# Kernel tuning notes

Measured on AMD Instinct MI355X. Metric: run time of the kernel, lower is better.

Reference implementation:

```python
import jax, jax.numpy as jnp
import numpy as np

N_NODES = 100000


def gcn_conv(x, edge_index, edge_weight, W, b):
    """PyG GCNConv: out = D^-1/2 (A + I) D^-1/2 X W + b (self-loop weight 1)."""
    n = x.shape[0]
    src, dst = edge_index[0], edge_index[1]
    loop = jnp.arange(n)
    src_sl = jnp.concatenate([src, loop])
    dst_sl = jnp.concatenate([dst, loop])
    ew_sl = jnp.concatenate([edge_weight, jnp.ones((n,), x.dtype)])
    deg = jax.ops.segment_sum(ew_sl, dst_sl, num_segments=n)  # [N]
    dinv = jnp.where(deg > 0, jax.lax.rsqrt(deg), 0.0)
    norm = dinv[src_sl] * ew_sl * dinv[dst_sl]  # [E+N]
    h = x @ W  # [N, out_dim] dense transform before propagation
    msg = h[src_sl] * norm[:, None]  # gather + scale, [E+N, out_dim]
    out = jax.ops.segment_sum(msg, dst_sl, num_segments=n)  # scatter-add
    return out + b


def setup_inputs() -> dict:
    key = jax.random.key(0)
    ks = jax.random.split(key, 9)
    in_dim, hidden, latent = 128, 64, 32
    n, e = N_NODES, 1600000
    x = jax.random.normal(ks[0], (n, in_dim), dtype=jnp.float32)
    edge_index = jax.random.randint(ks[1], (2, e), 0, n, dtype=jnp.int64)
    edge_weight = jax.random.uniform(ks[2], (e,), dtype=jnp.float32)
    def glorot(k, fan_in, fan_out):
        s = jnp.sqrt(6.0 / (fan_in + fan_out))
        return jax.random.uniform(k, (fan_in, fan_out), jnp.float32, -s, s)
    return {
        "x": x,
        "edge_index": edge_index,
        "edge_weight": edge_weight,
        "W1": glorot(ks[3], in_dim, hidden),
        "b1": jnp.zeros((hidden,), jnp.float32),
        "W_mu": glorot(ks[4], hidden, latent),
        "b_mu": jnp.zeros((latent,), jnp.float32),
        "W_lv": glorot(ks[5], hidden, latent),
        "b_lv": jnp.zeros((latent,), jnp.float32),
    }


def reference(x, edge_index, edge_weight, W1, b1, W_mu, b_mu, W_lv, b_lv):
    h = jax.nn.relu(gcn_conv(x, edge_index, edge_weight, W1, b1))
    mu = gcn_conv(h, edge_index, edge_weight, W_mu, b_mu)
    logvar = gcn_conv(h, edge_index, edge_weight, W_lv, b_lv)
    return (mu, logvar)
```

## Files before the change

kernel.cpp:

```cpp
#include <hip/hip_runtime.h>

static __device__ __forceinline__ float4 ld4(const float* p) { return *(const float4*)p; }
static __device__ __forceinline__ float b2f(unsigned short u) {
    return __uint_as_float((unsigned)u << 16);
}
static __device__ __forceinline__ float b2f_lo(unsigned u) { return __uint_as_float(u << 16); }
static __device__ __forceinline__ float b2f_hi(unsigned u) { return __uint_as_float(u & 0xFFFF0000u); }
static __device__ __forceinline__ unsigned short f2b(float f) {
    unsigned x = __float_as_uint(f);
    return (unsigned short)((x + 0x7FFFu + ((x >> 16) & 1u)) >> 16);
}
static __device__ __forceinline__ unsigned pk2(float lo, float hi) {
    return (unsigned)f2b(lo) | ((unsigned)f2b(hi) << 16);
}

typedef __attribute__((ext_vector_type(8))) short bf16x8;
typedef __attribute__((ext_vector_type(4))) float f32x4;

#define NPB 256
#define CAPE 5120



__global__ __launch_bounds__(256) void k_prep(const float* __restrict__ W1,
                                              const float* __restrict__ Wmu,
                                              const float* __restrict__ Wlv,
                                              unsigned short* __restrict__ Wf1,
                                              unsigned short* __restrict__ Wf2) {
    int tid = threadIdx.x;
    if (blockIdx.x == 0) {
        for (int idx = tid; idx < 2048; idx += 256) {
            int frag = idx >> 6, lane = idx & 63;
            int s = frag & 1, ct = (frag >> 1) & 3, kb = frag >> 3;
            int rA = lane & 15, g8 = (lane >> 4) * 8;
            int c = ct * 16 + rA;
            unsigned short* dstp = Wf1 + frag * 512 + lane * 8;
            for (int j = 0; j < 8; j++) {
                float wv = W1[(size_t)(kb * 32 + g8 + j) * 64 + c];
                unsigned short hi = f2b(wv);
                dstp[j] = (s == 0) ? hi : f2b(wv - b2f(hi));
            }
        }
    } else {
        for (int idx = tid; idx < 1024; idx += 256) {
            int frag = idx >> 6, lane = idx & 63;
            int s = frag & 1, ct = (frag >> 1) & 3, kb = frag >> 3;
            int rA = lane & 15, g8 = (lane >> 4) * 8;
            int c = ct * 16 + rA;
            int k0 = kb * 32 + g8;
            unsigned short* dstp = Wf2 + frag * 512 + lane * 8;
            for (int j = 0; j < 8; j++) {
                float wv = (c < 32) ? Wmu[(size_t)(k0 + j) * 32 + c]
                                    : Wlv[(size_t)(k0 + j) * 32 + (c - 32)];
                unsigned short hi = f2b(wv);
                dstp[j] = (s == 0) ? hi : f2b(wv - b2f(hi));
            }
        }
    }
}

static __device__ __forceinline__ void split8(const float* xv, bf16x8& ah, bf16x8& al) {
    #pragma unroll
    for (int j = 0; j < 8; j++) {
        unsigned u = __float_as_uint(xv[j]);
        float res = xv[j] - __uint_as_float(u & 0xFFFF0000u);
        ah[j] = (short)(u >> 16);
        al[j] = (short)(__float_as_uint(res) >> 16);
    }
}

__global__ __launch_bounds__(256) void k_fused1(const float* __restrict__ A,
                                                const unsigned short* __restrict__ Wf1,
                                                unsigned short* __restrict__ gout,
                                                const int* __restrict__ src,
                                                const int* __restrict__ dst,
                                                const float* __restrict__ ew,
                                                int* __restrict__ bin_cnt,
                                                unsigned long long* __restrict__ ebuf,
                                                int n, int E, int bb_cnt, int NB) {
    __shared__ int hist[512];
    __shared__ int hbase[512];
    int tid = threadIdx.x;

    if ((int)blockIdx.x >= bb_cnt) {
        int row0 = ((int)blockIdx.x - bb_cnt) * 128;
        int w = tid >> 6, lane = tid & 63;
        int rA = lane & 15, g8 = (lane >> 4) * 8;
        int rowa = row0 + w * 16 + rA;
        int rowb = rowa + 64;
        const float* xa = A + (size_t)min(rowa, n - 1) * 128;
        const float* xb = A + (size_t)min(rowb, n - 1) * 128;
        f32x4 acc0[4] = {{0.f,0.f,0.f,0.f},{0.f,0.f,0.f,0.f},{0.f,0.f,0.f,0.f},{0.f,0.f,0.f,0.f}};
        f32x4 acc1[4] = {{0.f,0.f,0.f,0.f},{0.f,0.f,0.f,0.f},{0.f,0.f,0.f,0.f},{0.f,0.f,0.f,0.f}};
        #pragma unroll
        for (int kb = 0; kb < 4; kb++) {
            float4 va0 = ld4(xa + kb * 32 + g8);
            float4 va1 = ld4(xa + kb * 32 + g8 + 4);
            float4 vb0 = ld4(xb + kb * 32 + g8);
            float4 vb1 = ld4(xb + kb * 32 + g8 + 4);
            float xva[8] = {va0.x, va0.y, va0.z, va0.w, va1.x, va1.y, va1.z, va1.w};
            float xvb[8] = {vb0.x, vb0.y, vb0.z, vb0.w, vb1.x, vb1.y, vb1.z, vb1.w};
            bf16x8 ahA, alA, ahB, alB;
            split8(xva, ahA, alA);
            split8(xvb, ahB, alB);
            const unsigned short* wb = Wf1 + (size_t)(kb * 8) * 512 + lane * 8;
            #pragma unroll
            for (int ct = 0; ct < 4; ct++) {
                bf16x8 bh = *(const bf16x8*)(wb + (ct * 2 + 0) * 512);
                bf16x8 bl = *(const bf16x8*)(wb + (ct * 2 + 1) * 512);
                acc0[ct] = __builtin_amdgcn_mfma_f32_16x16x32_bf16(ahA, bh, acc0[ct], 0, 0, 0);
                acc0[ct] = __builtin_amdgcn_mfma_f32_16x16x32_bf16(alA, bh, acc0[ct], 0, 0, 0);
                acc0[ct] = __builtin_amdgcn_mfma_f32_16x16x32_bf16(ahA, bl, acc0[ct], 0, 0, 0);
                acc1[ct] = __builtin_amdgcn_mfma_f32_16x16x32_bf16(ahB, bh, acc1[ct], 0, 0, 0);
                acc1[ct] = __builtin_amdgcn_mfma_f32_16x16x32_bf16(alB, bh, acc1[ct], 0, 0, 0);
                acc1[ct] = __builtin_amdgcn_mfma_f32_16x16x32_bf16(ahB, bl, acc1[ct], 0, 0, 0);
            }
        }
        int rbase = row0 + w * 16 + (lane >> 4) * 4;
        #pragma unroll
        for (int reg = 0; reg < 4; reg++) {
            int grow = rbase + reg;
            if (grow < n) {
                #pragma unroll
                for (int ct = 0; ct < 4; ct++)
                    gout[(size_t)grow * 64 + ct * 16 + rA] = f2b(acc0[ct][reg]);
            }
            int grow2 = grow + 64;
            if (grow2 < n) {
                #pragma unroll
                for (int ct = 0; ct < 4; ct++)
                    gout[(size_t)grow2 * 64 + ct * 16 + rA] = f2b(acc1[ct][reg]);
            }
        }
    } else {
        for (int j = tid; j < NB; j += 256) hist[j] = 0;
        __syncthreads();
        int e0 = (int)blockIdx.x * 4096;
        unsigned long long pk[16]; int bb[16]; int loc[16];
        #pragma unroll
        for (int j = 0; j < 16; j++) {
            int e = e0 + j * 256 + tid;
            if (e < E) {
                int s = src[e];
                int d = dst[e];
                float w = ew[e];
                bb[j] = d >> 8;
                pk[j] = ((unsigned long long)__float_as_uint(w) << 32) |
                        (unsigned)((d & (NPB - 1)) << 17) | (unsigned)s;
                loc[j] = atomicAdd(&hist[bb[j]], 1);
            } else bb[j] = -1;
        }
        __syncthreads();
        for (int j = tid; j < NB; j += 256) hbase[j] = atomicAdd(&bin_cnt[j], hist[j]);
        __syncthreads();
        #pragma unroll
        for (int j = 0; j < 16; j++) {
            if (bb[j] >= 0)
                ebuf[(size_t)bb[j] * CAPE + hbase[bb[j]] + loc[j]] = pk[j];
        }
    }
}

__global__ __launch_bounds__(512) void k_csr_build(const unsigned long long* __restrict__ ebuf,
                                                   const int* __restrict__ bin_cnt,
                                                   int2* __restrict__ rowcnt,
                                                   float* __restrict__ dinv,
                                                   unsigned long long* __restrict__ csr,
                                                   int n) {
    __shared__ unsigned long long eL[CAPE];
    __shared__ unsigned cntL[NPB];
    __shared__ unsigned ewsL[NPB];
    __shared__ unsigned fillL[NPB];
    __shared__ int scanL[512];
    __shared__ int rowL[NPB];
    __shared__ int binbase_s;
    int b = blockIdx.x;
    int tid = threadIdx.x;
    if (tid < NPB) { cntL[tid] = 0; ewsL[tid] = 0; fillL[tid] = 0; }
    scanL[tid] = (tid < b) ? bin_cnt[tid] : 0;
    __syncthreads();
    int m = bin_cnt[b];
    const unsigned long long* eb = ebuf + (size_t)b * CAPE;
    for (int i = tid; i < m; i += 512) {
        unsigned long long pk = eb[i];
        eL[i] = pk;
        int ld = (int)((pk >> 17) & (NPB - 1));
        float w = __uint_as_float((unsigned)(pk >> 32));
        atomicAdd(&cntL[ld], 1u);
        atomicAdd(&ewsL[ld], (unsigned)(w * 16777216.0f));
    }
    __syncthreads();
    #pragma unroll
    for (int off = 256; off > 0; off >>= 1) {
        if (tid < off) scanL[tid] += scanL[tid + off];
        __syncthreads();
    }
    if (tid == 0) binbase_s = scanL[0];
    __syncthreads();
    int v = (tid < NPB) ? (int)cntL[tid] : 0;
    scanL[tid] = v;
    __syncthreads();
    #pragma unroll
    for (int off = 1; off < 512; off <<= 1) {
        int t = (tid >= off) ? scanL[tid - off] : 0;
        __syncthreads();
        scanL[tid] += t;
        __syncthreads();
    }
    if (tid < NPB) {
        int rp = binbase_s + scanL[tid] - v;
        rowL[tid] = rp;
        int node = b * NPB + tid;
        if (node < n) {
            rowcnt[node] = make_int2(rp, v);
            dinv[node] = rsqrtf(1.0f + (float)ewsL[tid] * (1.0f / 16777216.0f));
        }
    }
    __syncthreads();
    for (int i = tid; i < m; i += 512) {
        unsigned long long pk = eL[i];
        int s = (int)(pk & 0x1FFFF);
        int ld = (int)((pk >> 17) & (NPB - 1));
        int pos = rowL[ld] + (int)atomicAdd(&fillL[ld], 1u);
        csr[pos] = (unsigned long long)(unsigned)s | (pk & 0xFFFFFFFF00000000ull);
    }
}

__global__ __launch_bounds__(256) void k_gemm2(const unsigned short* __restrict__ h,
                                               const unsigned short* __restrict__ Wf2,
                                               const float* __restrict__ dinv,
                                               unsigned short* __restrict__ out, int n) {
    int tid = threadIdx.x;
    int row0 = blockIdx.x * 128;
    int w = tid >> 6, lane = tid & 63;
    int rA = lane & 15, g8 = (lane >> 4) * 8;
    int rowa = row0 + w * 16 + rA;
    int rowb = rowa + 64;
    const unsigned short* ha = h + (size_t)min(rowa, n - 1) * 64;
    const unsigned short* hb = h + (size_t)min(rowb, n - 1) * 64;
    f32x4 acc0[4] = {{0.f,0.f,0.f,0.f},{0.f,0.f,0.f,0.f},{0.f,0.f,0.f,0.f},{0.f,0.f,0.f,0.f}};
    f32x4 acc1[4] = {{0.f,0.f,0.f,0.f},{0.f,0.f,0.f,0.f},{0.f,0.f,0.f,0.f},{0.f,0.f,0.f,0.f}};
    #pragma unroll
    for (int kb = 0; kb < 2; kb++) {
        bf16x8 aA = *(const bf16x8*)(ha + kb * 32 + g8);
        bf16x8 aB = *(const bf16x8*)(hb + kb * 32 + g8);
        const unsigned short* wb = Wf2 + (size_t)(kb * 8) * 512 + lane * 8;
        #pragma unroll
        for (int ct = 0; ct < 4; ct++) {
            bf16x8 bh = *(const bf16x8*)(wb + (ct * 2 + 0) * 512);
            bf16x8 bl = *(const bf16x8*)(wb + (ct * 2 + 1) * 512);
            acc0[ct] = __builtin_amdgcn_mfma_f32_16x16x32_bf16(aA, bh, acc0[ct], 0, 0, 0);
            acc0[ct] = __builtin_amdgcn_mfma_f32_16x16x32_bf16(aA, bl, acc0[ct], 0, 0, 0);
            acc1[ct] = __builtin_amdgcn_mfma_f32_16x16x32_bf16(aB, bh, acc1[ct], 0, 0, 0);
            acc1[ct] = __builtin_amdgcn_mfma_f32_16x16x32_bf16(aB, bl, acc1[ct], 0, 0, 0);
        }
    }
    int rbase = row0 + w * 16 + (lane >> 4) * 4;
    #pragma unroll
    for (int reg = 0; reg < 4; reg++) {
        int grow = rbase + reg;
        if (grow < n) {
            float sc = dinv[grow];
            #pragma unroll
            for (int ct = 0; ct < 4; ct++)
                out[(size_t)grow * 64 + ct * 16 + rA] = f2b(acc0[ct][reg] * sc);
        }
        int grow2 = grow + 64;
        if (grow2 < n) {
            float sc = dinv[grow2];
            #pragma unroll
            for (int ct = 0; ct < 4; ct++)
                out[(size_t)grow2 * 64 + ct * 16 + rA] = f2b(acc1[ct][reg] * sc);
        }
    }
}

static __device__ __forceinline__ void acc8(float* a, uint4 r, float wt) {
    a[0] = fmaf(b2f_lo(r.x), wt, a[0]); a[1] = fmaf(b2f_hi(r.x), wt, a[1]);
    a[2] = fmaf(b2f_lo(r.y), wt, a[2]); a[3] = fmaf(b2f_hi(r.y), wt, a[3]);
    a[4] = fmaf(b2f_lo(r.z), wt, a[4]); a[5] = fmaf(b2f_hi(r.z), wt, a[5]);
    a[6] = fmaf(b2f_lo(r.w), wt, a[6]); a[7] = fmaf(b2f_hi(r.w), wt, a[7]);
}

template<bool RELU, bool SPLIT_OUT, bool DSCALE>
__global__ __launch_bounds__(256) void k_prop(const unsigned short* __restrict__ g,
                                              const int2* __restrict__ csr,
                                              const int2* __restrict__ rowcnt,
                                              const float* __restrict__ dinv,
                                              const float* __restrict__ bias0,
                                              const float* __restrict__ bias1,
                                              void* __restrict__ outv, int n) {
    int node = blockIdx.x * 4 + (threadIdx.x >> 6);
    if (node >= n) return;
    int lane = threadIdx.x & 63;
    int q = lane >> 3;
    int t = lane & 7;
    uint4 sr = *(const uint4*)(g + (size_t)node * 64 + t * 8);
    int2 rc = rowcnt[node];
    const int2* ep = csr + rc.x;
    int m = rc.y;
    float a[8] = {};
    if (m > 0 && m <= 16) {
        int e1 = q, e2 = q + 8;
        int i1 = min(e1, m - 1), i2 = min(e2, m - 1);
        int2 p1 = ep[i1];
        int2 p2 = ep[i2];
        uint4 r1 = *(const uint4*)(g + (size_t)p1.x * 64 + t * 8);
        uint4 r2 = *(const uint4*)(g + (size_t)p2.x * 64 + t * 8);
        float w1 = (e1 < m) ? __int_as_float(p1.y) : 0.f;
        float w2 = (e2 < m) ? __int_as_float(p2.y) : 0.f;
        if (DSCALE) { w1 *= dinv[p1.x]; w2 *= dinv[p2.x]; }
        acc8(a, r1, w1);
        acc8(a, r2, w2);
    } else {
        for (int e = 0; e < m; e += 32) {
            int e1 = e + q, e2 = e1 + 8, e3 = e1 + 16, e4 = e1 + 24;
            int i1 = min(e1, m - 1), i2 = min(e2, m - 1);
            int i3 = min(e3, m - 1), i4 = min(e4, m - 1);
            int2 p1 = ep[i1];
            int2 p2 = ep[i2];
            int2 p3 = ep[i3];
            int2 p4 = ep[i4];
            uint4 r1 = *(const uint4*)(g + (size_t)p1.x * 64 + t * 8);
            uint4 r2 = *(const uint4*)(g + (size_t)p2.x * 64 + t * 8);
            uint4 r3 = *(const uint4*)(g + (size_t)p3.x * 64 + t * 8);
            uint4 r4 = *(const uint4*)(g + (size_t)p4.x * 64 + t * 8);
            float w1 = (e1 < m) ? __int_as_float(p1.y) : 0.f;
            float w2 = (e2 < m) ? __int_as_float(p2.y) : 0.f;
            float w3 = (e3 < m) ? __int_as_float(p3.y) : 0.f;
            float w4 = (e4 < m) ? __int_as_float(p4.y) : 0.f;
            if (DSCALE) {
                w1 *= dinv[p1.x]; w2 *= dinv[p2.x];
                w3 *= dinv[p3.x]; w4 *= dinv[p4.x];
            }
            acc8(a, r1, w1);
            acc8(a, r2, w2);
            acc8(a, r3, w3);
            acc8(a, r4, w4);
        }
    }
    #pragma unroll
    for (int i = 0; i < 8; i++) {
        a[i] += __shfl_xor(a[i], 8);
        a[i] += __shfl_xor(a[i], 16);
        a[i] += __shfl_xor(a[i], 32);
    }
    if (q != 0) return;
    float di = dinv[node];
    float ss = DSCALE ? di : 1.f;
    a[0] += ss * b2f_lo(sr.x); a[1] += ss * b2f_hi(sr.x);
    a[2] += ss * b2f_lo(sr.y); a[3] += ss * b2f_hi(sr.y);
    a[4] += ss * b2f_lo(sr.z); a[5] += ss * b2f_hi(sr.z);
    a[6] += ss * b2f_lo(sr.w); a[7] += ss * b2f_hi(sr.w);
    #pragma unroll
    for (int i = 0; i < 8; i++) a[i] *= di;
    if (!SPLIT_OUT) {
        float4 b0 = ld4(bias0 + t * 8);
        float4 b1 = ld4(bias0 + t * 8 + 4);
        a[0] += b0.x; a[1] += b0.y; a[2] += b0.z; a[3] += b0.w;
        a[4] += b1.x; a[5] += b1.y; a[6] += b1.z; a[7] += b1.w;
        if (RELU) {
            #pragma unroll
            for (int i = 0; i < 8; i++) a[i] = fmaxf(a[i], 0.f);
        }
        uint4 u = make_uint4(pk2(a[0], a[1]), pk2(a[2], a[3]),
                             pk2(a[4], a[5]), pk2(a[6], a[7]));
        *(uint4*)((unsigned short*)outv + (size_t)node * 64 + t * 8) = u;
    } else {
        float* out = (float*)outv;
        const float* bp = (t < 4) ? (bias0 + t * 8) : (bias1 + (t - 4) * 8);
        size_t base = (t < 4) ? ((size_t)node * 32 + t * 8)
                              : ((size_t)n * 32 + (size_t)node * 32 + (t - 4) * 8);
        float4 b0 = ld4(bp);
        float4 b1 = ld4(bp + 4);
        float4 v0 = make_float4(a[0] + b0.x, a[1] + b0.y, a[2] + b0.z, a[3] + b0.w);
        float4 v1 = make_float4(a[4] + b1.x, a[5] + b1.y, a[6] + b1.z, a[7] + b1.w);
        *(float4*)&out[base] = v0;
        *(float4*)&out[base + 4] = v1;
    }
}

extern "C" void kernel_launch(void* const* d_in, const int* in_sizes, int n_in,
                              void* d_out, int out_size, void* d_ws, size_t ws_size,
                              hipStream_t stream) {
    const float* x   = (const float*)d_in[0];
    const int*   ei  = (const int*)d_in[1];
    const float* ew  = (const float*)d_in[2];
    const float* W1  = (const float*)d_in[3];
    const float* b1  = (const float*)d_in[4];
    const float* Wmu = (const float*)d_in[5];
    const float* bmu = (const float*)d_in[6];
    const float* Wlv = (const float*)d_in[7];
    const float* blv = (const float*)d_in[8];
    float* outp = (float*)d_out;

    const int n = in_sizes[0] / 128;
    const int E = in_sizes[2];
    const int* src = ei;
    const int* dst = ei + E;
    const int NB = (n + NPB - 1) / NPB;

    size_t o = 0;
    auto alloc = [&](size_t bytes) { void* p = (char*)d_ws + o; o += (bytes + 511) & ~(size_t)511; return p; };
    int*   bin_cnt  = (int*)alloc((size_t)NB * 4);
    int2*  rowcnt   = (int2*)alloc((size_t)n * 8);
    float* dinv     = (float*)alloc((size_t)n * 4);
    unsigned long long* csr  = (unsigned long long*)alloc((size_t)E * 8);
    unsigned long long* ebuf = (unsigned long long*)alloc((size_t)NB * CAPE * 8);
    unsigned short* g0 = (unsigned short*)alloc((size_t)n * 64 * 2);
    unsigned short* h  = (unsigned short*)alloc((size_t)n * 64 * 2);
    unsigned short* Wf1 = (unsigned short*)alloc(32 * 512 * 2);
    unsigned short* Wf2 = (unsigned short*)alloc(16 * 512 * 2);
    unsigned short* g2 = g0;

    const int gb = (n + 127) / 128;
    const int bb = (E + 4095) / 4096;

    k_prep<<<2, 256, 0, stream>>>(W1, Wmu, Wlv, Wf1, Wf2);
    hipMemsetAsync(bin_cnt, 0, (size_t)NB * 4, stream);
    k_fused1<<<bb + gb, 256, 0, stream>>>(x, Wf1, g0, src, dst, ew,
                                          bin_cnt, ebuf, n, E, bb, NB);
    k_csr_build<<<NB, 512, 0, stream>>>(ebuf, bin_cnt, rowcnt, dinv, csr, n);
    k_prop<true, false, true><<<(n + 3) / 4, 256, 0, stream>>>(g0, (const int2*)csr, rowcnt, dinv,
                                                               b1, nullptr, h, n);
    k_gemm2<<<(n + 127) / 128, 256, 0, stream>>>(h, Wf2, dinv, g2, n);
    k_prop<false, true, false><<<(n + 3) / 4, 256, 0, stream>>>(g2, (const int2*)csr, rowcnt, dinv,
                                                                bmu, blv, outp, n);
}
```

Measured before the change: 273.0 us.

## Interleave GEMM and edge-binning blocks in fused kernel with smaller GEMM tiles

Halves the GEMM tile from 128 to 64 rows per block and interleaves GEMM blocks with edge-binning blocks (4 GEMM : 1 binning per group of 5), so the memory-bound binning work runs alongside compute instead of after it. It also software-prefetches the next k-slice of x before processing the current one. Costs are more blocks, each reloading the W fragments, some idle early-exit blocks when the two counts don't match, and lower per-block reuse.

```diff
diff --git a/kernel.cpp b/kernel.cpp
--- a/kernel.cpp
+++ b/kernel.cpp
@@ -77,44 +77,43 @@
                                                 const float* __restrict__ ew,
                                                 int* __restrict__ bin_cnt,
                                                 unsigned long long* __restrict__ ebuf,
-                                                int n, int E, int bb_cnt, int NB) {
+                                                int n, int E, int gb, int bb_cnt, int NB) {
     __shared__ int hist[512];
     __shared__ int hbase[512];
     int tid = threadIdx.x;
-
-    if ((int)blockIdx.x >= bb_cnt) {
-        int row0 = ((int)blockIdx.x - bb_cnt) * 128;
+    int bid = blockIdx.x;
+
+    if ((bid % 5) != 4) {
+        int gi = (bid / 5) * 4 + (bid % 5);
+        if (gi >= gb) return;
+        int row0 = gi * 64;
         int w = tid >> 6, lane = tid & 63;
         int rA = lane & 15, g8 = (lane >> 4) * 8;
-        int rowa = row0 + w * 16 + rA;
-        int rowb = rowa + 64;
-        const float* xa = A + (size_t)min(rowa, n - 1) * 128;
-        const float* xb = A + (size_t)min(rowb, n - 1) * 128;
-        f32x4 acc0[4] = {{0.f,0.f,0.f,0.f},{0.f,0.f,0.f,0.f},{0.f,0.f,0.f,0.f},{0.f,0.f,0.f,0.f}};
-        f32x4 acc1[4] = {{0.f,0.f,0.f,0.f},{0.f,0.f,0.f,0.f},{0.f,0.f,0.f,0.f},{0.f,0.f,0.f,0.f}};
+        int row = row0 + w * 16 + rA;
+        const float* xr = A + (size_t)min(row, n - 1) * 128;
+        f32x4 acc[4] = {{0.f,0.f,0.f,0.f},{0.f,0.f,0.f,0.f},{0.f,0.f,0.f,0.f},{0.f,0.f,0.f,0.f}};
+        float4 c0 = ld4(xr + g8);
+        float4 c1 = ld4(xr + g8 + 4);
         #pragma unroll
         for (int kb = 0; kb < 4; kb++) {
-            float4 va0 = ld4(xa + kb * 32 + g8);
-            float4 va1 = ld4(xa + kb * 32 + g8 + 4);
-            float4 vb0 = ld4(xb + kb * 32 + g8);
-            float4 vb1 = ld4(xb + kb * 32 + g8 + 4);
-            float xva[8] = {va0.x, va0.y, va0.z, va0.w, va1.x, va1.y, va1.z, va1.w};
-            float xvb[8] = {vb0.x, vb0.y, vb0.z, vb0.w, vb1.x, vb1.y, vb1.z, vb1.w};
-            bf16x8 ahA, alA, ahB, alB;
-            split8(xva, ahA, alA);
-            split8(xvb, ahB, alB);
+            float4 n0, n1;
+            if (kb < 3) {
+                n0 = ld4(xr + (kb + 1) * 32 + g8);
+                n1 = ld4(xr + (kb + 1) * 32 + g8 + 4);
+            }
+            float xv[8] = {c0.x, c0.y, c0.z, c0.w, c1.x, c1.y, c1.z, c1.w};
+            bf16x8 ah, al;
+            split8(xv, ah, al);
             const unsigned short* wb = Wf1 + (size_t)(kb * 8) * 512 + lane * 8;
             #pragma unroll
             for (int ct = 0; ct < 4; ct++) {
                 bf16x8 bh = *(const bf16x8*)(wb + (ct * 2 + 0) * 512);
                 bf16x8 bl = *(const bf16x8*)(wb + (ct * 2 + 1) * 512);
-                acc0[ct] = __builtin_amdgcn_mfma_f32_16x16x32_bf16(ahA, bh, acc0[ct], 0, 0, 0);
-                acc0[ct] = __builtin_amdgcn_mfma_f32_16x16x32_bf16(alA, bh, acc0[ct], 0, 0, 0);
-                acc0[ct] = __builtin_amdgcn_mfma_f32_16x16x32_bf16(ahA, bl, acc0[ct], 0, 0, 0);
-                acc1[ct] = __builtin_amdgcn_mfma_f32_16x16x32_bf16(ahB, bh, acc1[ct], 0, 0, 0);
-                acc1[ct] = __builtin_amdgcn_mfma_f32_16x16x32_bf16(alB, bh, acc1[ct], 0, 0, 0);
-                acc1[ct] = __builtin_amdgcn_mfma_f32_16x16x32_bf16(ahB, bl, acc1[ct], 0, 0, 0);
-            }
+                acc[ct] = __builtin_amdgcn_mfma_f32_16x16x32_bf16(ah, bh, acc[ct], 0, 0, 0);
+                acc[ct] = __builtin_amdgcn_mfma_f32_16x16x32_bf16(al, bh, acc[ct], 0, 0, 0);
+                acc[ct] = __builtin_amdgcn_mfma_f32_16x16x32_bf16(ah, bl, acc[ct], 0, 0, 0);
+            }
+            if (kb < 3) { c0 = n0; c1 = n1; }
         }
         int rbase = row0 + w * 16 + (lane >> 4) * 4;
         #pragma unroll
@@ -123,19 +122,15 @@
             if (grow < n) {
                 #pragma unroll
                 for (int ct = 0; ct < 4; ct++)
-                    gout[(size_t)grow * 64 + ct * 16 + rA] = f2b(acc0[ct][reg]);
-            }
-            int grow2 = grow + 64;
-            if (grow2 < n) {
-                #pragma unroll
-                for (int ct = 0; ct < 4; ct++)
-                    gout[(size_t)grow2 * 64 + ct * 16 + rA] = f2b(acc1[ct][reg]);
+                    gout[(size_t)grow * 64 + ct * 16 + rA] = f2b(acc[ct][reg]);
             }
         }
     } else {
+        int bi = bid / 5;
+        if (bi >= bb_cnt) return;
         for (int j = tid; j < NB; j += 256) hist[j] = 0;
         __syncthreads();
-        int e0 = (int)blockIdx.x * 4096;
+        int e0 = bi * 4096;
         unsigned long long pk[16]; int bb[16]; int loc[16];
         #pragma unroll
         for (int j = 0; j < 16; j++) {
@@ -413,13 +408,14 @@
     unsigned short* Wf2 = (unsigned short*)alloc(16 * 512 * 2);
     unsigned short* g2 = g0;
 
-    const int gb = (n + 127) / 128;
+    const int gb = (n + 63) / 64;
     const int bb = (E + 4095) / 4096;
+    const int groups = max(bb, (gb + 3) / 4);
 
     k_prep<<<2, 256, 0, stream>>>(W1, Wmu, Wlv, Wf1, Wf2);
     hipMemsetAsync(bin_cnt, 0, (size_t)NB * 4, stream);
-    k_fused1<<<bb + gb, 256, 0, stream>>>(x, Wf1, g0, src, dst, ew,
-                                          bin_cnt, ebuf, n, E, bb, NB);
+    k_fused1<<<groups * 5, 256, 0, stream>>>(x, Wf1, g0, src, dst, ew,
+                                             bin_cnt, ebuf, n, E, gb, bb, NB);
     k_csr_build<<<NB, 512, 0, stream>>>(ebuf, bin_cnt, rowcnt, dinv, csr, n);
     k_prop<true, false, true><<<(n + 3) / 4, 256, 0, stream>>>(g0, (const int2*)csr, rowcnt, dinv,
                                                                b1, nullptr, h, n);
```

Result: no change. 274.1 us (+0.4%).
